# Kernel tuning notes

Hardware: AMD Instinct MI355X
Metric: run time of the kernel (lower is better)

## Reference

```python
import jax, jax.numpy as jnp
import numpy as np

WINDOW = 3
FILTER = 6
FEATURE = 768
SEQ = 256
PAD = WINDOW // 2


def setup_inputs() -> dict:
    key = jax.random.key(0)
    k1, k2, k3 = jax.random.split(key, 3)
    B = 256
    inputs = jax.random.normal(k1, (B, SEQ, FEATURE), dtype=jnp.float32)
    # per-position Linear weights: torch nn.Linear stores [out, in]; we keep [S, in, out]
    bound = 1.0 / np.sqrt(WINDOW * FEATURE)
    W = jax.random.uniform(k2, (SEQ, WINDOW * FEATURE, FILTER), dtype=jnp.float32,
                           minval=-bound, maxval=bound)
    b = jax.random.uniform(k3, (SEQ, FILTER), dtype=jnp.float32,
                           minval=-bound, maxval=bound)
    return {"inputs": inputs, "W": W, "b": b}


def reference(inputs, W, b):
    # inputs: [B, S, F]. Pad along sequence with zeros (matches F.pad on transposed tensor).
    padded = jnp.pad(inputs, ((0, 0), (PAD, PAD), (0, 0)))  # [B, S+2p, F]
    # Vectorized sliding-window gather: idx [S, W]
    idx = jnp.arange(SEQ)[:, None] + jnp.arange(WINDOW)[None, :]
    windows = padded[:, idx, :]                              # [B, S, W, F]
    Bsz = windows.shape[0]
    windows = windows.reshape(Bsz, SEQ, WINDOW * FEATURE)    # [B, S, W*F]
    # Per-position distinct Linear + ReLU (Dropout is identity at inference)
    out = jnp.einsum('bsf,sfo->bso', windows, W) + b[None, :, :]
    return jax.nn.relu(out)
```

## Files before the change

kernel.cpp:

```cpp
#include <hip/hip_runtime.h>

#define SEQ    256
#define FEAT   768
#define WIN    3
#define FILT   6
#define KTOT   (WIN * FEAT)
#define WELEMS (KTOT * FILT)
#define NCHUNK (WELEMS / 24)
#define CSTR4  7
#define NB     8
#define BLOCK  1024
#define NWAVES (BLOCK / 64)
#define BATCH  256
#define NGROUPS (BATCH / NB)

__global__ __launch_bounds__(BLOCK, 4)
void pos_linear_kernel(const float* __restrict__ x,
                       const float* __restrict__ W,
                       const float* __restrict__ bias,
                       float* __restrict__ out) {
    __shared__ float4 wlds4[NCHUNK * CSTR4];
    const int s   = blockIdx.x;
    const int tid = threadIdx.x;

    {
        const float4* src = (const float4*)(W + (size_t)s * WELEMS);
        for (int i = tid; i < WELEMS / 4; i += BLOCK) {
            const int c = i / 6, j = i - c * 6;
            wlds4[c * CSTR4 + j] = src[i];
        }
    }
    __syncthreads();

    const int lane = tid & 63;
    const int wave = tid >> 6;

    for (int g = wave; g < NGROUPS; g += NWAVES) {
        const int b0 = g * NB;

        float acc[NB][FILT];
        #pragma unroll
        for (int nb = 0; nb < NB; ++nb)
            #pragma unroll
            for (int o = 0; o < FILT; ++o) acc[nb][o] = 0.f;

        #pragma unroll
        for (int w = 0; w < WIN; ++w) {
            const int r = s - 1 + w;
            if (r < 0 || r >= SEQ) continue;
            const float* xrow0 = x + ((size_t)b0 * SEQ + r) * FEAT;

            for (int i = 0; i < FEAT / 256; ++i) {
                const int f4 = lane + 64 * i;

                float4 wv4[6];
                {
                    const float4* wc = wlds4 + (size_t)(w * (FEAT / 4) + f4) * CSTR4;
                    #pragma unroll
                    for (int rr = 0; rr < 6; ++rr) wv4[rr] = wc[rr];
                }
                const float* wv = (const float*)wv4;

                float4 xv[NB];
                #pragma unroll
                for (int nb = 0; nb < NB; ++nb)
                    xv[nb] = *(const float4*)(xrow0 + (size_t)nb * SEQ * FEAT + 4 * f4);

                #pragma unroll
                for (int nb = 0; nb < NB; ++nb) {
                    const float* xf = (const float*)&xv[nb];
                    #pragma unroll
                    for (int ff = 0; ff < 4; ++ff)
                        #pragma unroll
                        for (int o = 0; o < FILT; ++o)
                            acc[nb][o] = fmaf(xf[ff], wv[ff * FILT + o], acc[nb][o]);
                }
            }
        }

        float v[NB * FILT];
        #pragma unroll
        for (int nb = 0; nb < NB; ++nb)
            #pragma unroll
            for (int o = 0; o < FILT; ++o) v[nb * FILT + o] = acc[nb][o];

        #pragma unroll
        for (int step = 0; step < 4; ++step) {
            const int m = 1 << step;
            const int half = 48 >> (step + 1);
            const bool upper = (lane & m) != 0;
            #pragma unroll
            for (int j = 0; j < half; ++j) {
                float snd = upper ? v[j] : v[j + half];
                float kep = upper ? v[j + half] : v[j];
                v[j] = kep + __shfl_xor(snd, m, 64);
            }
        }
        #pragma unroll
        for (int j = 0; j < 3; ++j) {
            v[j] += __shfl_xor(v[j], 16, 64);
            v[j] += __shfl_xor(v[j], 32, 64);
        }

        if (lane < 16) {
            const int gidx = ((lane & 1) << 3) | ((lane & 2) << 1) |
                             ((lane & 4) >> 1) | ((lane & 8) >> 3);
            #pragma unroll
            for (int j = 0; j < 3; ++j) {
                const int idx = 3 * gidx + j;
                const int nb  = idx / FILT;
                const int o   = idx - nb * FILT;
                float r0 = v[j] + bias[s * FILT + o];
                r0 = r0 > 0.f ? r0 : 0.f;
                out[((size_t)(b0 + nb) * SEQ + s) * FILT + o] = r0;
            }
        }
    }
}

extern "C" void kernel_launch(void* const* d_in, const int* in_sizes, int n_in,
                              void* d_out, int out_size, void* d_ws, size_t ws_size,
                              hipStream_t stream) {
    const float* x   = (const float*)d_in[0];
    const float* W   = (const float*)d_in[1];
    const float* b   = (const float*)d_in[2];
    float*       out = (float*)d_out;
    (void)in_sizes; (void)n_in; (void)out_size; (void)d_ws; (void)ws_size;
    pos_linear_kernel<<<SEQ, BLOCK, 0, stream>>>(x, W, b, out);
}
```

Before: 348.0 us.

## Split K across waves with LDS cross-wave reduction and swizzled block order

Work is repartitioned so that each of 12 waves owns one window row and a quarter of the features, and every wave walks all batch groups. Partial sums are combined across waves in double-buffered LDS, with one barrier per group. The weight LDS layout drops its padding, and the block index is remapped so neighbouring sequence positions run on different blocks. The goal is better balance and sharing of the x rows, at the cost of scalar x loads instead of float4 and an extra barrier every group.

```diff
diff --git a/kernel.cpp b/kernel.cpp
--- a/kernel.cpp
+++ b/kernel.cpp
@@ -1,92 +1,81 @@
 #include <hip/hip_runtime.h>
 
-#define SEQ    256
-#define FEAT   768
-#define WIN    3
-#define FILT   6
-#define KTOT   (WIN * FEAT)
-#define WELEMS (KTOT * FILT)
-#define NCHUNK (WELEMS / 24)
-#define CSTR4  7
-#define NB     8
-#define BLOCK  1024
-#define NWAVES (BLOCK / 64)
-#define BATCH  256
-#define NGROUPS (BATCH / NB)
+#define SEQ     256
+#define FEAT    768
+#define WIN     3
+#define FILT    6
+#define KTOT    (WIN * FEAT)
+#define WELEMS  (KTOT * FILT)
+#define NB      8
+#define BLOCK   768
+#define NWAVES  12
+#define NGROUPS 32
+#define RSTR    49
 
-__global__ __launch_bounds__(BLOCK, 4)
+__global__ __launch_bounds__(BLOCK, 3)
 void pos_linear_kernel(const float* __restrict__ x,
                        const float* __restrict__ W,
                        const float* __restrict__ bias,
                        float* __restrict__ out) {
-    __shared__ float4 wlds4[NCHUNK * CSTR4];
-    const int s   = blockIdx.x;
+    __shared__ float wlds[WELEMS];
+    __shared__ float red[2][NWAVES * RSTR];
+
+    const int blk = blockIdx.x;
+    const int s   = ((blk & 7) << 5) | (blk >> 3);
     const int tid = threadIdx.x;
 
     {
         const float4* src = (const float4*)(W + (size_t)s * WELEMS);
-        for (int i = tid; i < WELEMS / 4; i += BLOCK) {
-            const int c = i / 6, j = i - c * 6;
-            wlds4[c * CSTR4 + j] = src[i];
-        }
+        float4*       dst = (float4*)wlds;
+        for (int i = tid; i < WELEMS / 4; i += BLOCK) dst[i] = src[i];
     }
-    __syncthreads();
 
     const int lane = tid & 63;
     const int wave = tid >> 6;
+    const int w    = wave >> 2;
+    const int q    = wave & 3;
+    const int r    = s - 1 + w;
+    const bool valid = (r >= 0) && (r < SEQ);
+    const int  f0   = 192 * q + lane;
+    const int  k0   = FEAT * w + f0;
+    const float* xrow = valid ? (x + (size_t)r * FEAT + f0) : x;
 
-    for (int g = wave; g < NGROUPS; g += NWAVES) {
+    const int gidx = ((lane & 1) << 3) | ((lane & 2) << 1) |
+                     ((lane & 4) >> 1) | ((lane & 8) >> 3);
+
+    __syncthreads();
+
+    for (int g = 0; g < NGROUPS; ++g) {
         const int b0 = g * NB;
 
-        float acc[NB][FILT];
+        float v[NB * FILT];
         #pragma unroll
-        for (int nb = 0; nb < NB; ++nb)
+        for (int i = 0; i < NB * FILT; ++i) v[i] = 0.f;
+
+        if (valid) {
             #pragma unroll
-            for (int o = 0; o < FILT; ++o) acc[nb][o] = 0.f;
+            for (int j = 0; j < 3; ++j) {
+                const int kj = k0 + 64 * j;
+                float wv[FILT];
+                #pragma unroll
+                for (int o = 0; o < FILT; ++o) wv[o] = wlds[kj * FILT + o];
 
-        #pragma unroll
-        for (int w = 0; w < WIN; ++w) {
-            const int r = s - 1 + w;
-            if (r < 0 || r >= SEQ) continue;
-            const float* xrow0 = x + ((size_t)b0 * SEQ + r) * FEAT;
-
-            for (int i = 0; i < FEAT / 256; ++i) {
-                const int f4 = lane + 64 * i;
-
-                float4 wv4[6];
-                {
-                    const float4* wc = wlds4 + (size_t)(w * (FEAT / 4) + f4) * CSTR4;
-                    #pragma unroll
-                    for (int rr = 0; rr < 6; ++rr) wv4[rr] = wc[rr];
-                }
-                const float* wv = (const float*)wv4;
-
-                float4 xv[NB];
+                float xv[NB];
                 #pragma unroll
                 for (int nb = 0; nb < NB; ++nb)
-                    xv[nb] = *(const float4*)(xrow0 + (size_t)nb * SEQ * FEAT + 4 * f4);
+                    xv[nb] = xrow[(size_t)(b0 + nb) * (SEQ * FEAT) + 64 * j];
 
                 #pragma unroll
-                for (int nb = 0; nb < NB; ++nb) {
-                    const float* xf = (const float*)&xv[nb];
+                for (int nb = 0; nb < NB; ++nb)
                     #pragma unroll
-                    for (int ff = 0; ff < 4; ++ff)
-                        #pragma unroll
-                        for (int o = 0; o < FILT; ++o)
-                            acc[nb][o] = fmaf(xf[ff], wv[ff * FILT + o], acc[nb][o]);
-                }
+                    for (int o = 0; o < FILT; ++o)
+                        v[nb * FILT + o] = fmaf(xv[nb], wv[o], v[nb * FILT + o]);
             }
         }
 
-        float v[NB * FILT];
-        #pragma unroll
-        for (int nb = 0; nb < NB; ++nb)
-            #pragma unroll
-            for (int o = 0; o < FILT; ++o) v[nb * FILT + o] = acc[nb][o];
-
         #pragma unroll
         for (int step = 0; step < 4; ++step) {
-            const int m = 1 << step;
+            const int m    = 1 << step;
             const int half = 48 >> (step + 1);
             const bool upper = (lane & m) != 0;
             #pragma unroll
@@ -102,18 +91,24 @@
             v[j] += __shfl_xor(v[j], 32, 64);
         }
 
+        float* rb = red[g & 1];
         if (lane < 16) {
-            const int gidx = ((lane & 1) << 3) | ((lane & 2) << 1) |
-                             ((lane & 4) >> 1) | ((lane & 8) >> 3);
             #pragma unroll
-            for (int j = 0; j < 3; ++j) {
-                const int idx = 3 * gidx + j;
-                const int nb  = idx / FILT;
-                const int o   = idx - nb * FILT;
-                float r0 = v[j] + bias[s * FILT + o];
-                r0 = r0 > 0.f ? r0 : 0.f;
-                out[((size_t)(b0 + nb) * SEQ + s) * FILT + o] = r0;
-            }
+            for (int j = 0; j < 3; ++j)
+                rb[wave * RSTR + 3 * gidx + j] = v[j];
+        }
+        __syncthreads();
+
+        const int ft = tid - ((g % NWAVES) << 6);
+        if (ft >= 0 && ft < 48) {
+            float sum = 0.f;
+            #pragma unroll
+            for (int vw = 0; vw < NWAVES; ++vw) sum += rb[vw * RSTR + ft];
+            const int nb = ft / FILT;
+            const int o  = ft - nb * FILT;
+            float val = sum + bias[s * FILT + o];
+            val = val > 0.f ? val : 0.f;
+            out[((size_t)(b0 + nb) * SEQ + s) * FILT + o] = val;
         }
     }
 }
```

New measurement: 321.9 us. -7.5%, faster.
